# Kernel tuning notes

Measured on AMD Instinct MI355X. Metric: run time of the kernel, lower is better.

## Reference

```python
import jax, jax.numpy as jnp
import numpy as np

CLIP_LIMIT = 40.0
GRID = (8, 8)
NUM_BINS = 256


def setup_inputs() -> dict:
    key = jax.random.key(0)
    # CLAHE expects image values in [0, 1]
    x = jax.random.uniform(key, (8, 3, 1024, 1024), dtype=jnp.float32)
    return {"x": x}


def _interp_coords(n_tiles, tile_size, length):
    """Per-pixel tile-pair indices and blend weight along one axis.

    Follows kornia's half-tile interpolation grid: pixels in the first/last
    half-tile use only the nearest tile LUT; interior pixels blend the two
    nearest tile LUTs with weights linear over a full tile span (denom 2*half-1).
    """
    half = tile_size // 2
    pos = jnp.arange(length)
    j = pos // half          # interpolation-tile row/col index (0 .. 2*n_tiles-1)
    p = pos % half           # offset within the half tile
    r0 = jnp.clip((j - 1) // 2, 0, n_tiles - 1)
    r1 = jnp.clip(r0 + 1, 0, n_tiles - 1)
    denom = float(2 * half - 1)
    w = jnp.where(j % 2 == 1, (2 * half - 1) - p, (half - 1) - p).astype(jnp.float32) / denom
    w = jnp.where(j == 0, 1.0, w)  # first half-tile: nearest LUT only
    return r0, r1, w


def _clahe(x):
    B, C, H, W = x.shape
    GH, GW = GRID
    th = -(-H // GH); th += th % 2   # even tile height (kornia even_tile_size=True)
    tw = -(-W // GW); tw += tw % 2
    Hp, Wp = th * GH, tw * GW
    xp = jnp.pad(x, ((0, 0), (0, 0), (0, Hp - H), (0, Wp - W)), mode='reflect') if (Hp > H or Wp > W) else x

    # tiles: B x C x GH x GW x th x tw
    tiles = xp.reshape(B, C, GH, th, GW, tw).transpose(0, 1, 2, 4, 3, 5)
    pixels = th * tw
    T = B * C * GH * GW

    # per-tile 256-bin histogram (histc over [0,1] -> floor(x*256), last bin closed)
    bins = jnp.clip((tiles * NUM_BINS).astype(jnp.int32), 0, NUM_BINS - 1).reshape(T, pixels)
    hist = jnp.zeros((T, NUM_BINS), jnp.float32).at[jnp.arange(T)[:, None], bins].add(1.0)

    # clip + uniform redistribution of the excess (kornia scheme)
    if CLIP_LIMIT > 0:
        max_val = max(CLIP_LIMIT * pixels // NUM_BINS, 1.0)
        hist = jnp.minimum(hist, max_val)
        clipped = pixels - hist.sum(axis=1)                 # excess per tile
        residual = jnp.mod(clipped, NUM_BINS)
        hist = hist + ((clipped - residual) / NUM_BINS)[:, None]
        hist = hist + (jnp.arange(NUM_BINS)[None, :] < residual[:, None]).astype(jnp.float32)

    # LUT from CDF, floored to emulate integer conversion
    lut_scale = (NUM_BINS - 1) / pixels
    lut = jnp.floor(jnp.clip(jnp.cumsum(hist, axis=1) * lut_scale, 0, NUM_BINS - 1))
    lut = lut.reshape(B, C, GH, GW, NUM_BINS)

    # per-pixel LUT lookup index (kornia uses (x*255).long())
    idx = jnp.clip((xp * 255.0).astype(jnp.int32), 0, 255)

    r0, r1, wy = _interp_coords(GH, th, Hp)
    c0, c1, wx = _interp_coords(GW, tw, Wp)

    b_i = jnp.arange(B)[:, None, None, None]
    ch_i = jnp.arange(C)[None, :, None, None]

    def g(ry, cx):
        # gather lut[b, c, ry(y), cx(x), idx[b,c,y,x]] -> (B, C, Hp, Wp)
        return lut[b_i, ch_i, ry[None, None, :, None], cx[None, None, None, :], idx]

    wy2 = wy[:, None]
    wx2 = wx[None, :]
    out = (wy2 * wx2 * g(r0, c0)
           + wy2 * (1.0 - wx2) * g(r0, c1)
           + (1.0 - wy2) * wx2 * g(r1, c0)
           + (1.0 - wy2) * (1.0 - wx2) * g(r1, c1))
    return out[..., :H, :W] / 255.0


def reference(x):
    return _clahe(x)
```

## Files before the change

### kernel.cpp

```cpp
#include <hip/hip_runtime.h>

#define NBINS 256
#define TILE  128
#define CLIPV 2560u

typedef float fx4 __attribute__((ext_vector_type(4)));

#define IDX_OFF (512 * 1024)

__global__ __launch_bounds__(256) void clahe_hist_lut(
        const float* __restrict__ x, unsigned char* __restrict__ lut8,
        unsigned int* __restrict__ idxw) {
    const int t   = blockIdx.x;
    const int tid = threadIdx.x;

    __shared__ unsigned int hs[NBINS * 8];
    __shared__ int          scan[2][NBINS];
    __shared__ unsigned int wsum[4];

    #pragma unroll
    for (int k = 0; k < 8; ++k) hs[k * NBINS + tid] = 0u;
    __syncthreads();

    const int tx = t & 7;
    const int ty = (t >> 3) & 7;
    const int bc = t >> 6;
    const size_t pbase = ((size_t)bc * 1024 + (size_t)ty * TILE) * 1024
                       + (size_t)tx * TILE;
    const float* base = x + pbase;

    const int sub    = tid & 7;
    const int lane32 = tid & 31;
    const int rgrp   = tid >> 5;
    #pragma unroll 4
    for (int rr = 0; rr < 16; ++rr) {
        const int row = rr * 8 + rgrp;
        const fx4 v = __builtin_nontemporal_load(
            (const fx4*)(base + (size_t)row * 1024 + lane32 * 4));
        const int b0 = min(max((int)(v.x * 256.0f), 0), 255);
        const int b1 = min(max((int)(v.y * 256.0f), 0), 255);
        const int b2 = min(max((int)(v.z * 256.0f), 0), 255);
        const int b3 = min(max((int)(v.w * 256.0f), 0), 255);
        atomicAdd(&hs[b0 * 8 + sub], 1u);
        atomicAdd(&hs[b1 * 8 + sub], 1u);
        atomicAdd(&hs[b2 * 8 + sub], 1u);
        atomicAdd(&hs[b3 * 8 + sub], 1u);
        const unsigned i0 = (unsigned)min(max((int)(v.x * 255.0f), 0), 255);
        const unsigned i1 = (unsigned)min(max((int)(v.y * 255.0f), 0), 255);
        const unsigned i2 = (unsigned)min(max((int)(v.z * 255.0f), 0), 255);
        const unsigned i3 = (unsigned)min(max((int)(v.w * 255.0f), 0), 255);
        idxw[(pbase + (size_t)row * 1024 + lane32 * 4) >> 2] =
            i0 | (i1 << 8) | (i2 << 16) | (i3 << 24);
    }
    __syncthreads();

    const uint4* hp = (const uint4*)(&hs[tid * 8]);
    const uint4 ha = hp[0], hb = hp[1];
    const unsigned int total = ha.x + ha.y + ha.z + ha.w
                             + hb.x + hb.y + hb.z + hb.w;
    const unsigned int hv = min(total, CLIPV);
    unsigned int e = total - hv;
    #pragma unroll
    for (int off = 32; off > 0; off >>= 1) e += __shfl_down(e, off, 64);
    if ((tid & 63) == 0) wsum[tid >> 6] = e;
    __syncthreads();
    const unsigned int E        = wsum[0] + wsum[1] + wsum[2] + wsum[3];
    const unsigned int add      = E >> 8;
    const unsigned int residual = E & 255u;
    const int h2 = (int)(hv + add + ((unsigned)tid < residual ? 1u : 0u));

    scan[0][tid] = h2;
    __syncthreads();
    int src = 0;
    #pragma unroll
    for (int off = 1; off < 256; off <<= 1) {
        int v = scan[src][tid];
        if (tid >= off) v += scan[src][tid - off];
        scan[src ^ 1][tid] = v;
        __syncthreads();
        src ^= 1;
    }
    const int cum = scan[src][tid];
    const float l = fminf((float)cum * (255.0f / 16384.0f), 255.0f);
    lut8[(size_t)t * NBINS + tid] = (unsigned char)floorf(l);
}

__global__ __launch_bounds__(256) void clahe_apply(
        const unsigned int* __restrict__ idxr,
        const unsigned char* __restrict__ lut8,
        float* __restrict__ out) {
    __shared__ unsigned int ptab[8 * NBINS];

    const int blk = blockIdx.x;
    const int bc  = blk >> 6;
    const int rg  = blk & 63;
    const int y0  = rg * 16;
    const int tid = threadIdx.x;

    const int j = y0 >> 6;
    int r0 = (j - 1) >> 1;
    r0 = min(max(r0, 0), 7);
    const int r1 = min(r0 + 1, 7);

    {
        const unsigned char* L0 = lut8 + (size_t)bc * 64 * NBINS + (size_t)r0 * 8 * NBINS;
        const unsigned char* L1 = lut8 + (size_t)bc * 64 * NBINS + (size_t)r1 * 8 * NBINS;
        unsigned a0[8], a1[8];
        #pragma unroll
        for (int c = 0; c < 8; ++c) {
            a0[c] = L0[c * NBINS + tid];
            a1[c] = L1[c * NBINS + tid];
        }
        #pragma unroll
        for (int c0 = 0; c0 < 8; ++c0) {
            const int c1 = min(c0 + 1, 7);
            ptab[c0 * NBINS + tid] =
                a0[c0] | (a0[c1] << 8) | (a1[c0] << 16) | (a1[c1] << 24);
        }
    }
    __syncthreads();

    int ock[4];
    float wxk[4];
    #pragma unroll
    for (int k = 0; k < 4; ++k) {
        const int xx = tid * 4 + k;
        const int jc = xx >> 6, pc = xx & 63;
        int c0 = (jc - 1) >> 1;
        c0 = min(max(c0, 0), 7);
        ock[k] = c0 * NBINS;
        wxk[k] = (jc == 0) ? 1.0f
               : (float)((jc & 1) ? (127 - pc) : (63 - pc)) / 127.0f;
    }

    const bool jzero = (j == 0);
    const bool jodd  = (j & 1);
    const size_t rowbase = ((size_t)bc * 1024 + (size_t)y0) * 1024 + tid * 4;

    #pragma unroll 4
    for (int r = 0; r < 16; ++r) {
        const int p = (y0 + r) & 63;
        const float wy = jzero ? 1.0f
                       : (float)(jodd ? (127 - p) : (63 - p)) / 127.0f;

        const unsigned pk = idxr[(rowbase + (size_t)r * 1024) >> 2];
        float res[4];
        #pragma unroll
        for (int k = 0; k < 4; ++k) {
            const unsigned id = (pk >> (8 * k)) & 0xffu;
            const unsigned e = ptab[ock[k] + id];
            const float g00 = (float)(e & 0xffu);
            const float g01 = (float)((e >> 8) & 0xffu);
            const float g10 = (float)((e >> 16) & 0xffu);
            const float g11 = (float)(e >> 24);
            const float wx = wxk[k];
            const float a = fmaf(wx, g00 - g01, g01);
            const float b = fmaf(wx, g10 - g11, g11);
            res[k] = fmaf(wy, a - b, b) * (1.0f / 255.0f);
        }
        const fx4 o4 = {res[0], res[1], res[2], res[3]};
        __builtin_nontemporal_store(
            o4, (fx4*)(out + rowbase + (size_t)r * 1024));
    }
}

extern "C" void kernel_launch(void* const* d_in, const int* in_sizes, int n_in,
                              void* d_out, int out_size, void* d_ws, size_t ws_size,
                              hipStream_t stream) {
    const float* x = (const float*)d_in[0];
    float* out = (float*)d_out;
    unsigned char* lut8 = (unsigned char*)d_ws;
    unsigned int*  idxw = (unsigned int*)((char*)d_ws + IDX_OFF);

    clahe_hist_lut<<<1536, 256, 0, stream>>>(x, lut8, idxw);
    clahe_apply<<<24 * 64, 256, 0, stream>>>(idxw, lut8, out);
}
```

Baseline: 180.0 us.

## Fuse histogram and apply into one cooperative kernel keeping indices in registers

Replaces the two-kernel pipeline with one cooperative kernel of 1024 persistent blocks. Each block builds LUTs for one or two tiles, holds the packed per-pixel LUT indices in registers, waits at a grid-wide barrier, then applies bilinear interpolation to the same tiles. This removes the write and re-read of the intermediate index buffer and one launch, at the cost of a grid sync, extra register pressure from the 32 held words, and uneven load because some blocks handle two tiles. If the cooperative launch fails, it falls back to the original two kernels.

```diff
diff --git a/kernel.cpp b/kernel.cpp
--- a/kernel.cpp
+++ b/kernel.cpp
@@ -1,12 +1,174 @@
 #include <hip/hip_runtime.h>
-
-#define NBINS 256
-#define TILE  128
-#define CLIPV 2560u
+#include <hip/hip_cooperative_groups.h>
+
+namespace cg = cooperative_groups;
+
+#define NBINS  256
+#define CLIPV  2560u
+#define NTILES 1536
+#define NBLK   1024
 
 typedef float fx4 __attribute__((ext_vector_type(4)));
 
 #define IDX_OFF (512 * 1024)
+
+__global__ __launch_bounds__(256, 4) void clahe_fused(
+        const float* __restrict__ x, unsigned char* __restrict__ lut8,
+        float* __restrict__ out) {
+    const int tid = threadIdx.x;
+    const int blk = blockIdx.x;
+
+    __shared__ unsigned int hs[NBINS * 8];
+    __shared__ int          sc[2][NBINS];
+    __shared__ unsigned int wsum[4];
+    __shared__ unsigned int ptab[4 * NBINS];
+
+    const int sub    = tid & 7;
+    const int lane32 = tid & 31;
+    const int rgrp   = tid >> 5;
+
+    unsigned idxA[16], idxB[16];
+
+    auto histTile = [&](int t, unsigned (&idxp)[16]) {
+        #pragma unroll
+        for (int k = 0; k < 8; ++k) hs[k * NBINS + tid] = 0u;
+        __syncthreads();
+
+        const int tx = t & 7, ty = (t >> 3) & 7, bc = t >> 6;
+        const float* base = x + ((size_t)bc * 1024 + (size_t)ty * 128) * 1024
+                              + (size_t)tx * 128;
+        #pragma unroll
+        for (int rr = 0; rr < 16; ++rr) {
+            const int row = rr * 8 + rgrp;
+            const fx4 v = __builtin_nontemporal_load(
+                (const fx4*)(base + (size_t)row * 1024 + lane32 * 4));
+            const int b0 = min(max((int)(v.x * 256.0f), 0), 255);
+            const int b1 = min(max((int)(v.y * 256.0f), 0), 255);
+            const int b2 = min(max((int)(v.z * 256.0f), 0), 255);
+            const int b3 = min(max((int)(v.w * 256.0f), 0), 255);
+            atomicAdd(&hs[b0 * 8 + sub], 1u);
+            atomicAdd(&hs[b1 * 8 + sub], 1u);
+            atomicAdd(&hs[b2 * 8 + sub], 1u);
+            atomicAdd(&hs[b3 * 8 + sub], 1u);
+            const unsigned i0 = (unsigned)min(max((int)(v.x * 255.0f), 0), 255);
+            const unsigned i1 = (unsigned)min(max((int)(v.y * 255.0f), 0), 255);
+            const unsigned i2 = (unsigned)min(max((int)(v.z * 255.0f), 0), 255);
+            const unsigned i3 = (unsigned)min(max((int)(v.w * 255.0f), 0), 255);
+            idxp[rr] = i0 | (i1 << 8) | (i2 << 16) | (i3 << 24);
+        }
+        __syncthreads();
+
+        const uint4* hp = (const uint4*)(&hs[tid * 8]);
+        const uint4 ha = hp[0], hb = hp[1];
+        const unsigned int total = ha.x + ha.y + ha.z + ha.w
+                                 + hb.x + hb.y + hb.z + hb.w;
+        const unsigned int hv = min(total, CLIPV);
+        unsigned int e = total - hv;
+        #pragma unroll
+        for (int off = 32; off > 0; off >>= 1) e += __shfl_down(e, off, 64);
+        if ((tid & 63) == 0) wsum[tid >> 6] = e;
+        __syncthreads();
+        const unsigned int E        = wsum[0] + wsum[1] + wsum[2] + wsum[3];
+        const unsigned int add      = E >> 8;
+        const unsigned int residual = E & 255u;
+        const int h2 = (int)(hv + add + ((unsigned)tid < residual ? 1u : 0u));
+
+        sc[0][tid] = h2;
+        __syncthreads();
+        int src = 0;
+        #pragma unroll
+        for (int off = 1; off < 256; off <<= 1) {
+            int v = sc[src][tid];
+            if (tid >= off) v += sc[src][tid - off];
+            sc[src ^ 1][tid] = v;
+            __syncthreads();
+            src ^= 1;
+        }
+        const int cum = sc[src][tid];
+        const float l = fminf((float)cum * (255.0f / 16384.0f), 255.0f);
+        lut8[(size_t)t * NBINS + tid] = (unsigned char)floorf(l);
+        __syncthreads();
+    };
+
+    auto applyTile = [&](int t, unsigned (&idxp)[16]) {
+        const int tx = t & 7, ty = (t >> 3) & 7, bc = t >> 6;
+
+        __syncthreads();
+        {
+            const unsigned char* lutP = lut8 + (size_t)bc * 64 * NBINS;
+            const int ra0 = max(ty - 1, 0), ra1 = min(ra0 + 1, 7);
+            const int rb0 = ty,             rb1 = min(ty + 1, 7);
+            const int ca0 = max(tx - 1, 0), ca1 = min(ca0 + 1, 7);
+            const int cb0 = tx,             cb1 = min(tx + 1, 7);
+            const int R0[2] = {ra0, rb0}, R1[2] = {ra1, rb1};
+            const int C0[2] = {ca0, cb0}, C1[2] = {ca1, cb1};
+            #pragma unroll
+            for (int rp = 0; rp < 2; ++rp)
+                #pragma unroll
+                for (int cp = 0; cp < 2; ++cp) {
+                    const unsigned g00 = lutP[(R0[rp] * 8 + C0[cp]) * NBINS + tid];
+                    const unsigned g01 = lutP[(R0[rp] * 8 + C1[cp]) * NBINS + tid];
+                    const unsigned g10 = lutP[(R1[rp] * 8 + C0[cp]) * NBINS + tid];
+                    const unsigned g11 = lutP[(R1[rp] * 8 + C1[cp]) * NBINS + tid];
+                    ptab[(rp * 2 + cp) * NBINS + tid] =
+                        g00 | (g01 << 8) | (g10 << 16) | (g11 << 24);
+                }
+        }
+        __syncthreads();
+
+        int   cbase[4];
+        float wxk[4];
+        #pragma unroll
+        for (int k = 0; k < 4; ++k) {
+            const int cx = lane32 * 4 + k;
+            const int cp = cx >> 6;
+            const int pc = cx & 63;
+            cbase[k] = cp * NBINS;
+            wxk[k] = (tx == 0 && cp == 0) ? 1.0f
+                   : (float)(cp ? (127 - pc) : (63 - pc)) / 127.0f;
+        }
+
+        float* obase = out + ((size_t)bc * 1024 + (size_t)ty * 128) * 1024
+                           + (size_t)tx * 128;
+        #pragma unroll
+        for (int rr = 0; rr < 16; ++rr) {
+            const int row = rr * 8 + rgrp;
+            const int rp  = (rr >= 8) ? 1 : 0;
+            const int p   = row & 63;
+            const float wy = (ty == 0 && rp == 0) ? 1.0f
+                           : (float)(rp ? (127 - p) : (63 - p)) / 127.0f;
+            const unsigned pk = idxp[rr];
+            float res[4];
+            #pragma unroll
+            for (int k = 0; k < 4; ++k) {
+                const unsigned id = (pk >> (8 * k)) & 0xffu;
+                const unsigned e = ptab[rp * (2 * NBINS) + cbase[k] + id];
+                const float g00 = (float)(e & 0xffu);
+                const float g01 = (float)((e >> 8) & 0xffu);
+                const float g10 = (float)((e >> 16) & 0xffu);
+                const float g11 = (float)(e >> 24);
+                const float wx = wxk[k];
+                const float a = fmaf(wx, g00 - g01, g01);
+                const float b = fmaf(wx, g10 - g11, g11);
+                res[k] = fmaf(wy, a - b, b) * (1.0f / 255.0f);
+            }
+            const fx4 o4 = {res[0], res[1], res[2], res[3]};
+            __builtin_nontemporal_store(
+                o4, (fx4*)(obase + (size_t)row * 1024 + lane32 * 4));
+        }
+    };
+
+    const bool has2 = (blk < NTILES - NBLK);
+
+    histTile(blk, idxA);
+    if (has2) histTile(blk + NBLK, idxB);
+
+    __threadfence();
+    cg::this_grid().sync();
+
+    applyTile(blk, idxA);
+    if (has2) applyTile(blk + NBLK, idxB);
+}
 
 __global__ __launch_bounds__(256) void clahe_hist_lut(
         const float* __restrict__ x, unsigned char* __restrict__ lut8,
@@ -25,8 +187,8 @@
     const int tx = t & 7;
     const int ty = (t >> 3) & 7;
     const int bc = t >> 6;
-    const size_t pbase = ((size_t)bc * 1024 + (size_t)ty * TILE) * 1024
-                       + (size_t)tx * TILE;
+    const size_t pbase = ((size_t)bc * 1024 + (size_t)ty * 128) * 1024
+                       + (size_t)tx * 128;
     const float* base = x + pbase;
 
     const int sub    = tid & 7;
@@ -170,8 +332,15 @@
     const float* x = (const float*)d_in[0];
     float* out = (float*)d_out;
     unsigned char* lut8 = (unsigned char*)d_ws;
-    unsigned int*  idxw = (unsigned int*)((char*)d_ws + IDX_OFF);
-
-    clahe_hist_lut<<<1536, 256, 0, stream>>>(x, lut8, idxw);
-    clahe_apply<<<24 * 64, 256, 0, stream>>>(idxw, lut8, out);
+
+    void* args[] = { (void*)&x, (void*)&lut8, (void*)&out };
+    hipError_t err = hipLaunchCooperativeKernel(
+        reinterpret_cast<const void*>(clahe_fused),
+        dim3(NBLK), dim3(256), args, 0, stream);
+
+    if (err != hipSuccess) {
+        unsigned int* idxw = (unsigned int*)((char*)d_ws + IDX_OFF);
+        clahe_hist_lut<<<1536, 256, 0, stream>>>(x, lut8, idxw);
+        clahe_apply<<<24 * 64, 256, 0, stream>>>(idxw, lut8, out);
+    }
 }
```

Measured after the change: 403.4 us. 124% more time.
